# Kernel optimization log

Measured on AMD Instinct MI355X. Metric: run time of the kernel, lower is better.

## Reference

```python
import jax, jax.numpy as jnp
import numpy as np

N_CELL, N_WELL = 200000, 512
E_CC, E_CW = 1600000, 65536
CF, WF, ED, H = 12, 8, 1, 64
NEG_SLOPE = 0.2


def _p(k, shape, fan_in):
    return jax.random.normal(k, shape, jnp.float32) * (1.0 / np.sqrt(fan_in))


def setup_inputs() -> dict:
    key = jax.random.key(0)
    ks = jax.random.split(key, 32)
    d = {}
    d['cell_x'] = jax.random.normal(ks[0], (N_CELL, CF), jnp.float32)
    d['well_x'] = jax.random.normal(ks[1], (N_WELL, WF), jnp.float32)
    d['c2c_edge_attr'] = jax.random.normal(ks[2], (E_CC, ED), jnp.float32)
    d['c2c_edge_index'] = jax.random.randint(ks[3], (2, E_CC), 0, N_CELL)
    cw_src = jax.random.randint(ks[4], (E_CW,), 0, N_CELL)
    cw_dst = jax.random.randint(ks[5], (E_CW,), 0, N_WELL)
    d['c2w_edge_index'] = jnp.stack([cw_src, cw_dst])
    d['W_cell_emb'] = _p(ks[6], (CF, H), CF)
    d['b_cell_emb'] = jnp.zeros((H,), jnp.float32)
    d['W_well_emb'] = _p(ks[7], (WF, H), WF)
    d['b_well_emb'] = jnp.zeros((H,), jnp.float32)
    d['W_edge_emb'] = _p(ks[8], (ED, H), ED)
    d['b_edge_emb'] = jnp.zeros((H,), jnp.float32)
    d['conv_lin'] = _p(ks[9], (3, H, H), H)
    d['conv_lin_edge'] = _p(ks[10], (3, H, H), H)
    d['conv_att_src'] = _p(ks[11], (3, H), H)
    d['conv_att_dst'] = _p(ks[12], (3, H), H)
    d['conv_att_edge'] = _p(ks[13], (3, H), H)
    d['conv_bias'] = jnp.zeros((3, H), jnp.float32)
    d['wc_lin'] = _p(ks[14], (H, H), H)
    d['wc_att_src'] = _p(ks[15], (H,), H)
    d['wc_att_dst'] = _p(ks[16], (H,), H)
    d['wc_bias'] = jnp.zeros((H,), jnp.float32)
    d['mlp_W1'] = _p(ks[17], (H, H), H)
    d['mlp_b1'] = jnp.zeros((H,), jnp.float32)
    d['mlp_W2'] = _p(ks[18], (H, 75), H)
    d['mlp_b2'] = jnp.zeros((75,), jnp.float32)
    return d


def segment_softmax(logits, seg, num_segments):
    m = jax.ops.segment_max(logits, seg, num_segments=num_segments)
    m = jnp.where(jnp.isfinite(m), m, 0.0)  # empty segments -> 0
    e = jnp.exp(logits - m[seg])
    s = jax.ops.segment_sum(e, seg, num_segments=num_segments)
    return e / s[seg]


def gat_layer(h_src, h_dst, src, dst, lin, att_s, att_d, bias, num_dst,
              edge_feat=None, lin_edge=None, att_e=None):
    # PyG GATConv, heads=1, concat=False, add_self_loops=False
    hs = h_src @ lin                      # [Ns, H]
    hd = hs if h_dst is h_src else h_dst @ lin
    alpha = (hs @ att_s)[src] + (hd @ att_d)[dst]  # [E]
    if edge_feat is not None:
        alpha = alpha + (edge_feat @ lin_edge) @ att_e
    alpha = jax.nn.leaky_relu(alpha, NEG_SLOPE)
    p = segment_softmax(alpha, dst, num_dst)       # scatter-softmax per dst
    out = jax.ops.segment_sum(hs[src] * p[:, None], dst, num_segments=num_dst)
    return out + bias


def reference(cell_x, well_x, c2c_edge_attr,
              W_cell_emb, b_cell_emb, W_well_emb, b_well_emb,
              W_edge_emb, b_edge_emb,
              conv_lin, conv_lin_edge, conv_att_src, conv_att_dst,
              conv_att_edge, conv_bias,
              wc_lin, wc_att_src, wc_att_dst, wc_bias,
              mlp_W1, mlp_b1, mlp_W2, mlp_b2,
              c2c_edge_index, c2w_edge_index):
    h_c = cell_x @ W_cell_emb + b_cell_emb
    h_w = well_x @ W_well_emb + b_well_emb
    ea = c2c_edge_attr @ W_edge_emb + b_edge_emb
    src, dst = c2c_edge_index[0], c2c_edge_index[1]
    n_cell = h_c.shape[0]
    for l in range(3):
        h_c = jax.nn.relu(
            gat_layer(h_c, h_c, src, dst, conv_lin[l], conv_att_src[l],
                      conv_att_dst[l], conv_bias[l], n_cell,
                      edge_feat=ea, lin_edge=conv_lin_edge[l],
                      att_e=conv_att_edge[l]))
    ws, wd = c2w_edge_index[0], c2w_edge_index[1]
    h_well = gat_layer(h_c, h_w, ws, wd, wc_lin, wc_att_src, wc_att_dst,
                       wc_bias, h_w.shape[0])
    out = jax.nn.relu(h_well @ mlp_W1 + mlp_b1) @ mlp_W2 + mlp_b2
    return out.reshape(-1, 3, 25)
```

## Files before the change

### kernel.cpp

```cpp
#include <hip/hip_runtime.h>
#include <hip/hip_fp16.h>
#include <math.h>

#define CCAP 32
#define OVF_CAP 8192

typedef __attribute__((ext_vector_type(8))) _Float16 f16x8;
typedef __attribute__((ext_vector_type(4))) float f32x4;

__device__ __forceinline__ float wsum(float v){
  #pragma unroll
  for (int o=32;o;o>>=1) v += __shfl_xor(v,o);
  return v;
}

__global__ void k_edge_scalars(const float* __restrict__ lin_edge,
                               const float* __restrict__ att_e,
                               const float* __restrict__ Wrow,
                               const float* __restrict__ bemb,
                               float* __restrict__ escal){
  int l = threadIdx.x >> 6, j = threadIdx.x & 63;
  float v = 0.f;
  for (int k=0;k<64;++k) v = fmaf(lin_edge[l*4096 + j*64 + k], att_e[l*64+k], v);
  float sv = wsum(Wrow[j]*v);
  float ov = wsum(bemb[j]*v);
  if (j==0){ escal[l]=sv; escal[3+l]=ov; }
}

__global__ void k_prepA(const float* __restrict__ W_cell, const float* __restrict__ b_cell,
                        const float* __restrict__ lin0, float* __restrict__ weff){
  int t = threadIdx.x;
  for (int o=t; o<832; o+=256){
    float acc = 0.f;
    if (o < 768){
      int r = o >> 6, c2 = o & 63;
      for (int c=0;c<64;++c) acc = fmaf(W_cell[r*64+c], lin0[c*64+c2], acc);
    } else {
      int c2 = o - 768;
      for (int c=0;c<64;++c) acc = fmaf(b_cell[c], lin0[c*64+c2], acc);
    }
    weff[o] = acc;
  }
}

__global__ void k_prepB(const float* __restrict__ W_well, const float* __restrict__ b_well,
                        const float* __restrict__ wc_lin, const float* __restrict__ att_d,
                        float* __restrict__ wprep){
  __shared__ float tmp[64];
  int t = threadIdx.x;
  if (t < 64){
    float a = 0.f;
    for (int c=0;c<64;++c) a = fmaf(wc_lin[t*64+c], att_d[c], a);
    tmp[t] = a;
  }
  __syncthreads();
  if (t < 9){
    float a = 0.f;
    if (t < 8){ for (int k=0;k<64;++k) a = fmaf(W_well[t*64+k], tmp[k], a); }
    else      { for (int k=0;k<64;++k) a = fmaf(b_well[k],     tmp[k], a); }
    wprep[t] = a;
  }
}

__global__ void k_well_ad2(const float* __restrict__ well_x, const float* __restrict__ wprep,
                           float* __restrict__ ad_w, int n){
  int w = blockIdx.x*blockDim.x + threadIdx.x;
  if (w >= n) return;
  float a = wprep[8];
  #pragma unroll
  for (int r=0;r<8;++r) a = fmaf(well_x[w*8+r], wprep[r], a);
  ad_w[w] = a;
}

__global__ void k_build_cc(const int* __restrict__ src, const int* __restrict__ dst,
                           const float* __restrict__ attr, int* __restrict__ deg,
                           int2* __restrict__ slot, int4* __restrict__ ovf,
                           int* __restrict__ n_ovf, int e){
  int stride = gridDim.x*blockDim.x;
  for (int i = blockIdx.x*blockDim.x + threadIdx.x; i < e; i += stride){
    int d = dst[i];
    int off = atomicAdd(&deg[d], 1);
    if (off < CCAP){
      slot[(d<<5) + off] = make_int2(src[i], __float_as_int(attr[i]));
    } else {
      int x = atomicAdd(n_ovf, 1);
      if (x < OVF_CAP) ovf[x] = make_int4(d, src[i], __float_as_int(attr[i]), 0);
    }
  }
}

__global__ void k_count_w(const int* __restrict__ dst, int* __restrict__ deg,
                          int* __restrict__ off, int e){
  int i = blockIdx.x*blockDim.x + threadIdx.x;
  if (i<e) off[i] = atomicAdd(&deg[dst[i]], 1);
}

__global__ void k_scan_single(const int* __restrict__ deg, int* __restrict__ rowptr, int n){
  __shared__ int sm[1024];
  int t = threadIdx.x;
  sm[t] = (t<n) ? deg[t] : 0; __syncthreads();
  for (int o=1;o<blockDim.x;o<<=1){
    int v = (t>=o)?sm[t-o]:0; __syncthreads();
    sm[t]+=v; __syncthreads();
  }
  if (t<n) rowptr[t+1]=sm[t];
  if (t==0) rowptr[0]=0;
}

__global__ void k_fill_w(const int* __restrict__ src, const int* __restrict__ dst,
                         const int* __restrict__ rowptr, const int* __restrict__ off,
                         int* __restrict__ slot, int e){
  int i = blockIdx.x*blockDim.x + threadIdx.x;
  if (i>=e) return;
  int d = dst[i];
  slot[rowptr[d] + off[i]] = src[i];
}

__global__ __launch_bounds__(256) void k_gemm64m(
    const __half* __restrict__ h, const float* __restrict__ W,
    const float* __restrict__ att_s, const float* __restrict__ att_d,
    __half* __restrict__ hs, float* __restrict__ as_, float* __restrict__ ad_, int n){
  __shared__ _Float16 hT[64][72];
  __shared__ _Float16 wT[64][72];
  int t = threadIdx.x;
  int n0 = blockIdx.x * 64;
  for (int i=t; i<1024; i+=256){
    int k = i >> 4, f4 = (i & 15) << 2;
    float4 w4 = *(const float4*)&W[k*64 + f4];
    wT[f4+0][k] = (_Float16)w4.x;
    wT[f4+1][k] = (_Float16)w4.y;
    wT[f4+2][k] = (_Float16)w4.z;
    wT[f4+3][k] = (_Float16)w4.w;
  }
  for (int i=t; i<512; i+=256){
    int node = i >> 3, c8 = (i & 7) << 3;
    int gn = n0 + node;
    if (gn < n){
      *(f16x8*)&hT[node][c8] = *(const f16x8*)&h[(size_t)gn*64 + c8];
    } else {
      f16x8 z = {0,0,0,0,0,0,0,0};
      *(f16x8*)&hT[node][c8] = z;
    }
  }
  __syncthreads();
  int w = t >> 6, lane = t & 63;
  int lr = lane & 15, lg = lane >> 4;
  f32x4 acc[4];
  #pragma unroll
  for (int c=0;c<4;++c) acc[c] = (f32x4){0.f,0.f,0.f,0.f};
  #pragma unroll
  for (int kk=0; kk<2; ++kk){
    f16x8 a = *(const f16x8*)&hT[16*w + lr][kk*32 + lg*8];
    #pragma unroll
    for (int c=0;c<4;++c){
      f16x8 b = *(const f16x8*)&wT[16*c + lr][kk*32 + lg*8];
      acc[c] = __builtin_amdgcn_mfma_f32_16x16x32_f16(a, b, acc[c], 0, 0, 0);
    }
  }
  float s_att[4], d_att[4];
  #pragma unroll
  for (int c=0;c<4;++c){ s_att[c]=att_s[16*c+lr]; d_att[c]=att_d[16*c+lr]; }
  #pragma unroll
  for (int r=0;r<4;++r){
    int gn = n0 + 16*w + lg*4 + r;
    float sv=0.f, dv=0.f;
    if (gn < n){
      #pragma unroll
      for (int c=0;c<4;++c){
        float v = acc[c][r];
        hs[(size_t)gn*64 + 16*c + lr] = __float2half(v);
        sv = fmaf(v, s_att[c], sv);
        dv = fmaf(v, d_att[c], dv);
      }
    }
    #pragma unroll
    for (int o=8;o;o>>=1){ sv += __shfl_xor(sv,o,16); dv += __shfl_xor(dv,o,16); }
    if (gn < n && lr==0){ as_[gn]=sv; ad_[gn]=dv; }
  }
}

__global__ __launch_bounds__(256) void k_gemm_l0(
    const float* __restrict__ x, const float* __restrict__ weff,
    const float* __restrict__ att_s, const float* __restrict__ att_d,
    __half* __restrict__ hs, float* __restrict__ as_, float* __restrict__ ad_, int n){
  __shared__ float Ws[12*64];
  __shared__ float xT[12][68];
  int t = threadIdx.x;
  int n0 = blockIdx.x * 64;
  for (int i=t;i<768;i+=256){
    Ws[i] = weff[i];
    int node = i / 12, r = i - node*12;
    int gn = n0 + node;
    xT[r][node] = (gn < n) ? x[(size_t)gn*12 + r] : 0.f;
  }
  __syncthreads();
  int tx = t & 15, ty = t >> 4;
  int f4 = tx*4;
  float4 be = *(const float4*)&weff[768 + f4];
  float acc[4][4];
  #pragma unroll
  for (int i=0;i<4;++i){ acc[i][0]=be.x; acc[i][1]=be.y; acc[i][2]=be.z; acc[i][3]=be.w; }
  #pragma unroll
  for (int k=0;k<12;++k){
    float4 wv = *(const float4*)&Ws[k*64 + f4];
    float hvv[4];
    #pragma unroll
    for (int i=0;i<4;++i) hvv[i] = xT[k][ty*4+i];
    float wvv[4] = {wv.x,wv.y,wv.z,wv.w};
    #pragma unroll
    for (int i=0;i<4;++i)
      #pragma unroll
      for (int j=0;j<4;++j)
        acc[i][j] = fmaf(hvv[i], wvv[j], acc[i][j]);
  }
  float4 s4 = *(const float4*)&att_s[f4];
  float4 d4 = *(const float4*)&att_d[f4];
  #pragma unroll
  for (int i=0;i<4;++i){
    int gn = n0 + ty*4 + i;
    if (gn < n){
      union { __half2 h2; unsigned u; } lo, hi;
      lo.h2 = __floats2half2_rn(acc[i][0], acc[i][1]);
      hi.h2 = __floats2half2_rn(acc[i][2], acc[i][3]);
      *(int2*)&hs[(size_t)gn*64 + f4] = make_int2((int)lo.u, (int)hi.u);
      float sv = acc[i][0]*s4.x + acc[i][1]*s4.y + acc[i][2]*s4.z + acc[i][3]*s4.w;
      float dv = acc[i][0]*d4.x + acc[i][1]*d4.y + acc[i][2]*d4.z + acc[i][3]*d4.w;
      #pragma unroll
      for (int o=8;o;o>>=1){ sv += __shfl_xor(sv,o); dv += __shfl_xor(dv,o); }
      if (tx==0){ as_[gn]=sv; ad_[gn]=dv; }
    }
  }
}

template<bool RELU>
__global__ __launch_bounds__(256) void k_gat_agg3(
    const int* __restrict__ deg, const int2* __restrict__ slot,
    const int4* __restrict__ ovf, const int* __restrict__ n_ovf_p,
    const float* __restrict__ as_, const float* __restrict__ ad_,
    const __half* __restrict__ hs, const float* __restrict__ bias,
    const float* __restrict__ escal, int l,
    __half* __restrict__ out, int n){
  int t = threadIdx.x;
  int g = t & 15;
  int node = blockIdx.x*16 + (t >> 4);
  if (node >= n) return;
  int degn = deg[node];
  float4 b4 = *(const float4*)&bias[g*4];
  if (degn == 0){
    float4 r = b4;
    if (RELU){ r.x=fmaxf(r.x,0.f); r.y=fmaxf(r.y,0.f); r.z=fmaxf(r.z,0.f); r.w=fmaxf(r.w,0.f); }
    union { __half2 h2[2]; int2 i2; } u;
    u.h2[0] = __floats2half2_rn(r.x, r.y);
    u.h2[1] = __floats2half2_rn(r.z, r.w);
    *(int2*)&out[(size_t)node*64 + g*4] = u.i2;
    return;
  }
  float se = escal[l], oe = escal[3+l];
  float adn = ad_[node];
  int cin = min(degn, CCAP);
  int sb = node << 5;
  float areg[2]; int sreg[2];
  float m = -1e30f;
  #pragma unroll
  for (int it=0; it<2; ++it){
    int k = it*16 + g;
    areg[it] = -1e30f; sreg[it] = 0;
    if (k < cin){
      int2 sv = slot[sb + k];
      float a = as_[sv.x] + adn;
      a = fmaf(__int_as_float(sv.y), se, a) + oe;
      a = (a >= 0.f) ? a : 0.2f*a;
      areg[it] = a; sreg[it] = sv.x;
      m = fmaxf(m, a);
    }
  }
  int no = 0;
  if (degn > CCAP) no = min(*n_ovf_p, OVF_CAP);
  for (int j=0;j<no;++j){
    int4 e = ovf[j];
    if (e.x == node){
      float a = as_[e.y] + adn;
      a = fmaf(__int_as_float(e.z), se, a) + oe;
      a = (a >= 0.f) ? a : 0.2f*a;
      m = fmaxf(m, a);
    }
  }
  #pragma unroll
  for (int o=8;o;o>>=1) m = fmaxf(m, __shfl_xor(m, o, 16));

  float sum = 0.f;
  float4 acc = make_float4(0.f,0.f,0.f,0.f);
  #pragma unroll
  for (int it=0; it<2; ++it){
    int base = it*16;
    if (base < cin){
      float p = (base + g < cin) ? __expf(areg[it] - m) : 0.f;
      sum += p;
      int cnt = min(16, cin - base);
      for (int j=0;j<cnt;j+=4){
        float pj[4]; int sj[4];
        int s0 = __shfl(sreg[it], j, 16);
        #pragma unroll
        for (int u=0;u<4;++u){
          int jj = j+u;
          bool act = (jj < cnt);
          pj[u] = act ? __shfl(p, jj, 16) : 0.f;
          int sv = __shfl(sreg[it], act ? jj : j, 16);
          sj[u] = act ? sv : s0;
        }
        int2 hb[4];
        #pragma unroll
        for (int u=0;u<4;++u) hb[u] = *(const int2*)&hs[(size_t)sj[u]*64 + g*4];
        #pragma unroll
        for (int u=0;u<4;++u){
          union { unsigned u32; __half2 h2; } a0, a1;
          a0.u32 = (unsigned)hb[u].x; a1.u32 = (unsigned)hb[u].y;
          float2 f0 = __half22float2(a0.h2);
          float2 f1 = __half22float2(a1.h2);
          acc.x = fmaf(f0.x, pj[u], acc.x);
          acc.y = fmaf(f0.y, pj[u], acc.y);
          acc.z = fmaf(f1.x, pj[u], acc.z);
          acc.w = fmaf(f1.y, pj[u], acc.w);
        }
      }
    }
  }
  for (int j=0;j<no;++j){
    int4 e = ovf[j];
    if (e.x == node){
      float a = as_[e.y] + adn;
      a = fmaf(__int_as_float(e.z), se, a) + oe;
      a = (a >= 0.f) ? a : 0.2f*a;
      float p = __expf(a - m);
      if (g == 0) sum += p;
      int2 hb = *(const int2*)&hs[(size_t)e.y*64 + g*4];
      union { unsigned u; __half2 h2; } a0, a1; a0.u = (unsigned)hb.x; a1.u = (unsigned)hb.y;
      float2 f0 = __half22float2(a0.h2);
      float2 f1 = __half22float2(a1.h2);
      acc.x = fmaf(f0.x, p, acc.x);
      acc.y = fmaf(f0.y, p, acc.y);
      acc.z = fmaf(f1.x, p, acc.z);
      acc.w = fmaf(f1.y, p, acc.w);
    }
  }
  #pragma unroll
  for (int o=8;o;o>>=1) sum += __shfl_xor(sum, o, 16);
  float4 r;
  r.x = acc.x/sum + b4.x;
  r.y = acc.y/sum + b4.y;
  r.z = acc.z/sum + b4.z;
  r.w = acc.w/sum + b4.w;
  if (RELU){ r.x=fmaxf(r.x,0.f); r.y=fmaxf(r.y,0.f); r.z=fmaxf(r.z,0.f); r.w=fmaxf(r.w,0.f); }
  union { __half2 h2[2]; int2 i2; } u;
  u.h2[0] = __floats2half2_rn(r.x, r.y);
  u.h2[1] = __floats2half2_rn(r.z, r.w);
  *(int2*)&out[(size_t)node*64 + g*4] = u.i2;
}

template<int NA>
__global__ __launch_bounds__(256) void k_gat_aggw(
    const int* __restrict__ rowptr, const int* __restrict__ slot1,
    float* __restrict__ alpha_ws,
    const float* __restrict__ as_, const float* __restrict__ ad_,
    const __half* __restrict__ hs, const float* __restrict__ bias,
    float* __restrict__ out, int n){
  int t = threadIdx.x;
  int g = t & 15;
  int node = blockIdx.x*16 + (t >> 4);
  if (node >= n) return;
  int beg = rowptr[node], end = rowptr[node+1];
  float4 b4 = *(const float4*)&bias[g*4];
  if (end == beg){
    *(float4*)&out[(size_t)node*64 + g*4] = b4;
    return;
  }
  float adn = ad_[node];
  float areg[NA]; int sreg[NA];
  float m = -1e30f;
  #pragma unroll
  for (int it=0; it<NA; ++it){
    int k = beg + it*16 + g;
    areg[it] = -1e30f; sreg[it] = 0;
    if (k < end){
      int s = slot1[k];
      float a = as_[s] + adn;
      a = (a >= 0.f) ? a : 0.2f*a;
      areg[it] = a; sreg[it] = s;
      m = fmaxf(m, a);
    }
  }
  for (int k = beg + NA*16 + g; k < end; k += 16){
    int s = slot1[k];
    float a = as_[s] + adn;
    a = (a >= 0.f) ? a : 0.2f*a;
    alpha_ws[k] = a;
    m = fmaxf(m, a);
  }
  #pragma unroll
  for (int o=8;o;o>>=1) m = fmaxf(m, __shfl_xor(m, o, 16));

  float sum = 0.f;
  float4 acc = make_float4(0.f,0.f,0.f,0.f);
  #pragma unroll
  for (int it=0; it<NA; ++it){
    int base = beg + it*16;
    if (base < end){
      float p = (base + g < end) ? __expf(areg[it] - m) : 0.f;
      sum += p;
      int cnt = min(16, end - base);
      for (int j=0;j<cnt;++j){
        float pj = __shfl(p, j, 16);
        int   sj = __shfl(sreg[it], j, 16);
        int2 hb = *(const int2*)&hs[(size_t)sj*64 + g*4];
        union { unsigned u; __half2 h2; } a0, a1; a0.u = (unsigned)hb.x; a1.u = (unsigned)hb.y;
        float2 f0 = __half22float2(a0.h2);
        float2 f1 = __half22float2(a1.h2);
        acc.x = fmaf(f0.x, pj, acc.x);
        acc.y = fmaf(f0.y, pj, acc.y);
        acc.z = fmaf(f1.x, pj, acc.z);
        acc.w = fmaf(f1.y, pj, acc.w);
      }
    }
  }
  for (int base = beg + NA*16; base < end; base += 16){
    int k = base + g;
    float p = 0.f; int s = 0;
    if (k < end){ s = slot1[k]; p = __expf(alpha_ws[k] - m); }
    sum += p;
    int cnt = min(16, end - base);
    for (int j=0;j<cnt;++j){
      float pj = __shfl(p, j, 16);
      int   sj = __shfl(s, j, 16);
      int2 hb = *(const int2*)&hs[(size_t)sj*64 + g*4];
      union { unsigned u; __half2 h2; } a0, a1; a0.u = (unsigned)hb.x; a1.u = (unsigned)hb.y;
      float2 f0 = __half22float2(a0.h2);
      float2 f1 = __half22float2(a1.h2);
      acc.x = fmaf(f0.x, pj, acc.x);
      acc.y = fmaf(f0.y, pj, acc.y);
      acc.z = fmaf(f1.x, pj, acc.z);
      acc.w = fmaf(f1.y, pj, acc.w);
    }
  }
  #pragma unroll
  for (int o=8;o;o>>=1) sum += __shfl_xor(sum, o, 16);
  float4 r;
  r.x = acc.x/sum + b4.x;
  r.y = acc.y/sum + b4.y;
  r.z = acc.z/sum + b4.z;
  r.w = acc.w/sum + b4.w;
  *(float4*)&out[(size_t)node*64 + g*4] = r;
}

__global__ __launch_bounds__(128) void k_mlp(const float* __restrict__ h_well,
    const float* __restrict__ W1, const float* __restrict__ b1,
    const float* __restrict__ W2, const float* __restrict__ b2,
    float* __restrict__ out, int n){
  __shared__ float hr[64]; __shared__ float h1[64];
  int w = blockIdx.x, t = threadIdx.x;
  if (t<64) hr[t] = h_well[w*64+t];
  __syncthreads();
  if (t<64){
    float a = b1[t];
    for (int k=0;k<64;++k) a = fmaf(hr[k], W1[k*64+t], a);
    h1[t] = fmaxf(a, 0.f);
  }
  __syncthreads();
  if (t<75){
    float a = b2[t];
    for (int k=0;k<64;++k) a = fmaf(h1[k], W2[k*75+t], a);
    out[w*75+t] = a;
  }
}

extern "C" void kernel_launch(void* const* d_in, const int* in_sizes, int n_in,
                              void* d_out, int out_size, void* d_ws, size_t ws_size,
                              hipStream_t stream){
  const float* cell_x = (const float*)d_in[0];
  const float* well_x = (const float*)d_in[1];
  const float* eattr  = (const float*)d_in[2];
  const int*   cc_idx = (const int*)d_in[3];
  const int*   cw_idx = (const int*)d_in[4];
  const float* W_cell = (const float*)d_in[5];
  const float* b_cell = (const float*)d_in[6];
  const float* W_well = (const float*)d_in[7];
  const float* b_well = (const float*)d_in[8];
  const float* W_edge = (const float*)d_in[9];
  const float* b_edge = (const float*)d_in[10];
  const float* conv_lin = (const float*)d_in[11];
  const float* conv_lin_edge = (const float*)d_in[12];
  const float* att_src = (const float*)d_in[13];
  const float* att_dst = (const float*)d_in[14];
  const float* att_edge = (const float*)d_in[15];
  const float* conv_bias = (const float*)d_in[16];
  const float* wc_lin = (const float*)d_in[17];
  const float* wc_att_src = (const float*)d_in[18];
  const float* wc_att_dst = (const float*)d_in[19];
  const float* wc_bias = (const float*)d_in[20];
  const float* mlp_W1 = (const float*)d_in[21];
  const float* mlp_b1 = (const float*)d_in[22];
  const float* mlp_W2 = (const float*)d_in[23];
  const float* mlp_b2 = (const float*)d_in[24];

  int n_cell = in_sizes[0]/12;
  int n_well = in_sizes[1]/8;
  int e_cc = in_sizes[2];
  int e_cw = in_sizes[4]/2;

  const int* cc_src = cc_idx;
  const int* cc_dst = cc_idx + e_cc;
  const int* cw_src = cw_idx;
  const int* cw_dst = cw_idx + e_cw;

  char* p = (char*)d_ws;
  auto alloc = [&](size_t bytes)->void*{
    void* r = (void*)p;
    p += (bytes + 255) & ~(size_t)255;
    return r;
  };
  __half* h_cur = (__half*)alloc((size_t)n_cell*64*2);
  __half* hs   = (__half*)alloc((size_t)n_cell*64*2);
  float* as_   = (float*)alloc((size_t)n_cell*4);
  float* ad_   = (float*)alloc((size_t)n_cell*4);
  int* deg     = (int*)alloc((size_t)n_cell*4);
  int2* slot2  = (int2*)alloc((size_t)n_cell*CCAP*8);
  int4* ovf    = (int4*)alloc((size_t)OVF_CAP*16);
  int* n_ovf   = (int*)alloc(256);
  float* ad_w  = (float*)alloc((size_t)n_well*4);
  int* wdeg    = (int*)alloc((size_t)n_well*4);
  int* wrowptr = (int*)alloc((size_t)(n_well+1)*4);
  int* woff    = (int*)alloc((size_t)e_cw*4);
  int* wslot   = (int*)alloc((size_t)e_cw*4);
  float* walpha= (float*)alloc((size_t)e_cw*4);
  float* h_well= (float*)alloc((size_t)n_well*64*4);
  float* escal = (float*)alloc(64);
  float* weff  = (float*)alloc(832*4);
  float* wprep = (float*)alloc(16*4);

  hipMemsetAsync(deg, 0, (size_t)n_cell*4, stream);
  hipMemsetAsync(wdeg, 0, (size_t)n_well*4, stream);
  hipMemsetAsync(n_ovf, 0, 4, stream);

  k_edge_scalars<<<1, 192, 0, stream>>>(conv_lin_edge, att_edge, W_edge, b_edge, escal);
  k_prepA<<<1, 256, 0, stream>>>(W_cell, b_cell, conv_lin, weff);
  k_prepB<<<1, 128, 0, stream>>>(W_well, b_well, wc_lin, wc_att_dst, wprep);

  int gB = (e_cc + 255)/256; if (gB > 2048) gB = 2048;
  k_build_cc<<<gB, 256, 0, stream>>>(cc_src, cc_dst, eattr, deg, slot2, ovf, n_ovf, e_cc);

  k_count_w<<<(e_cw+255)/256, 256, 0, stream>>>(cw_dst, wdeg, woff, e_cw);
  k_scan_single<<<1, 512, 0, stream>>>(wdeg, wrowptr, n_well);
  k_fill_w<<<(e_cw+255)/256, 256, 0, stream>>>(cw_src, cw_dst, wrowptr, woff, wslot, e_cw);

  k_gemm_l0<<<(n_cell+63)/64, 256, 0, stream>>>(cell_x, weff,
      att_src, att_dst, hs, as_, ad_, n_cell);
  k_gat_agg3<true><<<(n_cell+15)/16, 256, 0, stream>>>(deg, slot2, ovf, n_ovf,
      as_, ad_, hs, conv_bias, escal, 0, h_cur, n_cell);

  for (int l=1;l<3;++l){
    k_gemm64m<<<(n_cell+63)/64, 256, 0, stream>>>(h_cur, conv_lin + l*4096,
        att_src + l*64, att_dst + l*64, hs, as_, ad_, n_cell);
    k_gat_agg3<true><<<(n_cell+15)/16, 256, 0, stream>>>(deg, slot2, ovf, n_ovf,
        as_, ad_, hs, conv_bias + l*64, escal, l, h_cur, n_cell);
  }

  k_gemm64m<<<(n_cell+63)/64, 256, 0, stream>>>(h_cur, wc_lin, wc_att_src, wc_att_dst,
      hs, as_, ad_, n_cell);
  k_well_ad2<<<(n_well+255)/256, 256, 0, stream>>>(well_x, wprep, ad_w, n_well);
  k_gat_aggw<16><<<(n_well+15)/16, 256, 0, stream>>>(wrowptr, wslot,
      walpha, as_, ad_w, hs, wc_bias, h_well, n_well);

  k_mlp<<<n_well, 128, 0, stream>>>(h_well, mlp_W1, mlp_b1, mlp_W2, mlp_b2, (float*)d_out, n_well);
}
```

Measured before the change: 534.1 us.

## Use MFMA for layer-0 embedding GEMM, widen gather unroll, fuse well ad

```diff
diff --git a/kernel.cpp b/kernel.cpp
--- a/kernel.cpp
+++ b/kernel.cpp
@@ -60,16 +60,6 @@
     else      { for (int k=0;k<64;++k) a = fmaf(b_well[k],     tmp[k], a); }
     wprep[t] = a;
   }
-}
-
-__global__ void k_well_ad2(const float* __restrict__ well_x, const float* __restrict__ wprep,
-                           float* __restrict__ ad_w, int n){
-  int w = blockIdx.x*blockDim.x + threadIdx.x;
-  if (w >= n) return;
-  float a = wprep[8];
-  #pragma unroll
-  for (int r=0;r<8;++r) a = fmaf(well_x[w*8+r], wprep[r], a);
-  ad_w[w] = a;
 }
 
 __global__ void k_build_cc(const int* __restrict__ src, const int* __restrict__ dst,
@@ -179,56 +169,62 @@
   }
 }
 
-__global__ __launch_bounds__(256) void k_gemm_l0(
+__global__ __launch_bounds__(256) void k_gemm_l0m(
     const float* __restrict__ x, const float* __restrict__ weff,
     const float* __restrict__ att_s, const float* __restrict__ att_d,
     __half* __restrict__ hs, float* __restrict__ as_, float* __restrict__ ad_, int n){
-  __shared__ float Ws[12*64];
-  __shared__ float xT[12][68];
+  __shared__ _Float16 xT[64][40];
+  __shared__ _Float16 wT[64][40];
   int t = threadIdx.x;
   int n0 = blockIdx.x * 64;
-  for (int i=t;i<768;i+=256){
-    Ws[i] = weff[i];
+  for (int i=t; i<768; i+=256){
     int node = i / 12, r = i - node*12;
     int gn = n0 + node;
-    xT[r][node] = (gn < n) ? x[(size_t)gn*12 + r] : 0.f;
+    xT[node][r] = (gn < n) ? (_Float16)x[(size_t)gn*12 + r] : (_Float16)0.f;
+  }
+  for (int i=t; i<1280; i+=256){
+    int node = i / 20, r = 12 + (i % 20);
+    xT[node][r] = (_Float16)0.f;
+  }
+  for (int i=t; i<768; i+=256){
+    int k = i >> 6, f = i & 63;
+    wT[f][k] = (_Float16)weff[i];
+  }
+  for (int i=t; i<1280; i+=256){
+    int f = i / 20, k = 12 + (i % 20);
+    wT[f][k] = (_Float16)0.f;
   }
   __syncthreads();
-  int tx = t & 15, ty = t >> 4;
-  int f4 = tx*4;
-  float4 be = *(const float4*)&weff[768 + f4];
-  float acc[4][4];
-  #pragma unroll
-  for (int i=0;i<4;++i){ acc[i][0]=be.x; acc[i][1]=be.y; acc[i][2]=be.z; acc[i][3]=be.w; }
-  #pragma unroll
-  for (int k=0;k<12;++k){
-    float4 wv = *(const float4*)&Ws[k*64 + f4];
-    float hvv[4];
+  int w = t >> 6, lane = t & 63;
+  int lr = lane & 15, lg = lane >> 4;
+  f32x4 acc[4];
+  f16x8 a = *(const f16x8*)&xT[16*w + lr][lg*8];
+  #pragma unroll
+  for (int c=0;c<4;++c){
+    f16x8 b = *(const f16x8*)&wT[16*c + lr][lg*8];
+    acc[c] = __builtin_amdgcn_mfma_f32_16x16x32_f16(a, b, (f32x4){0.f,0.f,0.f,0.f}, 0, 0, 0);
+  }
+  float s_att[4], d_att[4], be[4];
+  #pragma unroll
+  for (int c=0;c<4;++c){
+    s_att[c]=att_s[16*c+lr]; d_att[c]=att_d[16*c+lr]; be[c]=weff[768 + 16*c + lr];
+  }
+  #pragma unroll
+  for (int r=0;r<4;++r){
+    int gn = n0 + 16*w + lg*4 + r;
+    float sv=0.f, dv=0.f;
+    if (gn < n){
+      #pragma unroll
+      for (int c=0;c<4;++c){
+        float v = acc[c][r] + be[c];
+        hs[(size_t)gn*64 + 16*c + lr] = __float2half(v);
+        sv = fmaf(v, s_att[c], sv);
+        dv = fmaf(v, d_att[c], dv);
+      }
+    }
     #pragma unroll
-    for (int i=0;i<4;++i) hvv[i] = xT[k][ty*4+i];
-    float wvv[4] = {wv.x,wv.y,wv.z,wv.w};
-    #pragma unroll
-    for (int i=0;i<4;++i)
-      #pragma unroll
-      for (int j=0;j<4;++j)
-        acc[i][j] = fmaf(hvv[i], wvv[j], acc[i][j]);
-  }
-  float4 s4 = *(const float4*)&att_s[f4];
-  float4 d4 = *(const float4*)&att_d[f4];
-  #pragma unroll
-  for (int i=0;i<4;++i){
-    int gn = n0 + ty*4 + i;
-    if (gn < n){
-      union { __half2 h2; unsigned u; } lo, hi;
-      lo.h2 = __floats2half2_rn(acc[i][0], acc[i][1]);
-      hi.h2 = __floats2half2_rn(acc[i][2], acc[i][3]);
-      *(int2*)&hs[(size_t)gn*64 + f4] = make_int2((int)lo.u, (int)hi.u);
-      float sv = acc[i][0]*s4.x + acc[i][1]*s4.y + acc[i][2]*s4.z + acc[i][3]*s4.w;
-      float dv = acc[i][0]*d4.x + acc[i][1]*d4.y + acc[i][2]*d4.z + acc[i][3]*d4.w;
-      #pragma unroll
-      for (int o=8;o;o>>=1){ sv += __shfl_xor(sv,o); dv += __shfl_xor(dv,o); }
-      if (tx==0){ as_[gn]=sv; ad_[gn]=dv; }
-    }
+    for (int o=8;o;o>>=1){ sv += __shfl_xor(sv,o,16); dv += __shfl_xor(dv,o,16); }
+    if (gn < n && lr==0){ as_[gn]=sv; ad_[gn]=dv; }
   }
 }
 
@@ -297,22 +293,22 @@
       float p = (base + g < cin) ? __expf(areg[it] - m) : 0.f;
       sum += p;
       int cnt = min(16, cin - base);
-      for (int j=0;j<cnt;j+=4){
-        float pj[4]; int sj[4];
+      for (int j=0;j<cnt;j+=8){
+        float pj[8]; int sj[8];
         int s0 = __shfl(sreg[it], j, 16);
         #pragma unroll
-        for (int u=0;u<4;++u){
+        for (int u=0;u<8;++u){
           int jj = j+u;
           bool act = (jj < cnt);
           pj[u] = act ? __shfl(p, jj, 16) : 0.f;
           int sv = __shfl(sreg[it], act ? jj : j, 16);
           sj[u] = act ? sv : s0;
         }
-        int2 hb[4];
+        int2 hb[8];
         #pragma unroll
-        for (int u=0;u<4;++u) hb[u] = *(const int2*)&hs[(size_t)sj[u]*64 + g*4];
+        for (int u=0;u<8;++u) hb[u] = *(const int2*)&hs[(size_t)sj[u]*64 + g*4];
         #pragma unroll
-        for (int u=0;u<4;++u){
+        for (int u=0;u<8;++u){
           union { unsigned u32; __half2 h2; } a0, a1;
           a0.u32 = (unsigned)hb[u].x; a1.u32 = (unsigned)hb[u].y;
           float2 f0 = __half22float2(a0.h2);
@@ -361,7 +357,8 @@
 __global__ __launch_bounds__(256) void k_gat_aggw(
     const int* __restrict__ rowptr, const int* __restrict__ slot1,
     float* __restrict__ alpha_ws,
-    const float* __restrict__ as_, const float* __restrict__ ad_,
+    const float* __restrict__ as_, const float* __restrict__ well_x,
+    const float* __restrict__ wprep,
     const __half* __restrict__ hs, const float* __restrict__ bias,
     float* __restrict__ out, int n){
   int t = threadIdx.x;
@@ -374,7 +371,9 @@
     *(float4*)&out[(size_t)node*64 + g*4] = b4;
     return;
   }
-  float adn = ad_[node];
+  float adn = wprep[8];
+  #pragma unroll
+  for (int r=0;r<8;++r) adn = fmaf(well_x[node*8+r], wprep[r], adn);
   float areg[NA]; int sreg[NA];
   float m = -1e30f;
   #pragma unroll
@@ -525,7 +524,6 @@
   int2* slot2  = (int2*)alloc((size_t)n_cell*CCAP*8);
   int4* ovf    = (int4*)alloc((size_t)OVF_CAP*16);
   int* n_ovf   = (int*)alloc(256);
-  float* ad_w  = (float*)alloc((size_t)n_well*4);
   int* wdeg    = (int*)alloc((size_t)n_well*4);
   int* wrowptr = (int*)alloc((size_t)(n_well+1)*4);
   int* woff    = (int*)alloc((size_t)e_cw*4);
@@ -551,7 +549,7 @@
   k_scan_single<<<1, 512, 0, stream>>>(wdeg, wrowptr, n_well);
   k_fill_w<<<(e_cw+255)/256, 256, 0, stream>>>(cw_src, cw_dst, wrowptr, woff, wslot, e_cw);
 
-  k_gemm_l0<<<(n_cell+63)/64, 256, 0, stream>>>(cell_x, weff,
+  k_gemm_l0m<<<(n_cell+63)/64, 256, 0, stream>>>(cell_x, weff,
       att_src, att_dst, hs, as_, ad_, n_cell);
   k_gat_agg3<true><<<(n_cell+15)/16, 256, 0, stream>>>(deg, slot2, ovf, n_ovf,
       as_, ad_, hs, conv_bias, escal, 0, h_cur, n_cell);
@@ -565,9 +563,8 @@
 
   k_gemm64m<<<(n_cell+63)/64, 256, 0, stream>>>(h_cur, wc_lin, wc_att_src, wc_att_dst,
       hs, as_, ad_, n_cell);
-  k_well_ad2<<<(n_well+255)/256, 256, 0, stream>>>(well_x, wprep, ad_w, n_well);
   k_gat_aggw<16><<<(n_well+15)/16, 256, 0, stream>>>(wrowptr, wslot,
-      walpha, as_, ad_w, hs, wc_bias, h_well, n_well);
+      walpha, as_, well_x, wprep, hs, wc_bias, h_well, n_well);
 
   k_mlp<<<n_well, 128, 0, stream>>>(h_well, mlp_W1, mlp_b1, mlp_W2, mlp_b2, (float*)d_out, n_well);
 }
```

After: 525.4 us. No clear change (-1.6%).
